# Kernel optimization log

Hardware: AMD Instinct MI355X
Metric: run time of the kernel (lower is better)

The kernel has to match this reference:

```python
import jax, jax.numpy as jnp
import numpy as np

B, N, E = 2, 2048, 1024
H = 16
D = E // H  # head_dim = 64
MLP = 4096
EPS = 1e-5


def _layernorm(x, g, b):
    mu = jnp.mean(x, axis=-1, keepdims=True)
    var = jnp.var(x, axis=-1, keepdims=True)
    return (x - mu) * jax.lax.rsqrt(var + EPS) * g + b


def setup_inputs() -> dict:
    key = jax.random.key(0)
    ks = jax.random.split(key, 12)
    s_e = 1.0 / np.sqrt(E)
    s_m = 1.0 / np.sqrt(MLP)
    return {
        "x": jax.random.normal(ks[0], (B, N, E), jnp.float32),
        "w_qkv": jax.random.uniform(ks[1], (E, 3 * E), jnp.float32, -s_e, s_e),
        "b_qkv": jax.random.uniform(ks[2], (3 * E,), jnp.float32, -s_e, s_e),
        "w_proj": jax.random.uniform(ks[3], (E, E), jnp.float32, -s_e, s_e),
        "b_proj": jax.random.uniform(ks[4], (E,), jnp.float32, -s_e, s_e),
        "g1": jnp.ones((E,), jnp.float32),
        "beta1": jnp.zeros((E,), jnp.float32),
        "g2": jnp.ones((E,), jnp.float32),
        "beta2": jnp.zeros((E,), jnp.float32),
        "w_fc1": jax.random.uniform(ks[5], (E, MLP), jnp.float32, -s_e, s_e),
        "b_fc1": jax.random.uniform(ks[6], (MLP,), jnp.float32, -s_e, s_e),
        "w_fc2": jax.random.uniform(ks[7], (MLP, E), jnp.float32, -s_m, s_m),
        "b_fc2": jax.random.uniform(ks[8], (E,), jnp.float32, -s_m, s_m),
    }


def reference(x, w_qkv, b_qkv, w_proj, b_proj, g1, beta1, g2, beta2,
              w_fc1, b_fc1, w_fc2, b_fc2):
    scale = D ** (-0.5)
    # --- attention block (pre-norm) ---
    h = _layernorm(x, g1, beta1)
    qkv = (h @ w_qkv + b_qkv).reshape(B, N, 3, H, D)
    q, k, v = (qkv[:, :, i].transpose(0, 2, 1, 3) for i in range(3))  # [B,H,N,D]
    scores = jnp.einsum("bhnd,bhmd->bhnm", q, k) * scale  # [B,H,N,N]
    attn = jax.nn.softmax(scores, axis=-1)
    out = jnp.einsum("bhnm,bhmd->bhnd", attn, v)
    out = out.transpose(0, 2, 1, 3).reshape(B, N, E)
    x = x + (out @ w_proj + b_proj)
    # --- MLP block (pre-norm, exact GELU as in torch default) ---
    h = _layernorm(x, g2, beta2)
    h = jax.nn.gelu(h @ w_fc1 + b_fc1, approximate=False) @ w_fc2 + b_fc2
    return x + h
```

## Files before the change

kernel.cpp:

```cpp
#include <hip/hip_runtime.h>
#include <hip/hip_bf16.h>
#include <cmath>


typedef __hip_bfloat16 bf16;
typedef __bf16 bf16x8 __attribute__((ext_vector_type(8)));
typedef __bf16 bf16x4v __attribute__((ext_vector_type(4)));
typedef float  f32x4  __attribute__((ext_vector_type(4)));

#define CB 2
#define CN 2048
#define CE 1024
#define CH 16
#define CD 64
#define CMLP 4096
#define CM (CB*CN)

#define PS 136

__device__ __forceinline__ float b2f(bf16 v){ return __bfloat162float(v); }
__device__ __forceinline__ bf16  f2b(float v){ return __float2bfloat16(v); }

__device__ __forceinline__ void gl_lds16(const void* g, void* l){
  __builtin_amdgcn_global_load_lds((__attribute__((address_space(1))) void*)g,
                                   (__attribute__((address_space(3))) void*)l,
                                   16, 0, 0);
}

__global__ __launch_bounds__(256) void transpose_k(const float* __restrict__ in,
                                                   bf16* __restrict__ out,
                                                   int K, int N){
  __shared__ float tile[32][33];
  const int n0 = blockIdx.x*32, k0 = blockIdx.y*32;
  const int tx = threadIdx.x & 31;
  const int ty = threadIdx.x >> 5;
  #pragma unroll
  for(int i=0;i<32;i+=8) tile[ty+i][tx] = in[(size_t)(k0+ty+i)*N + n0+tx];
  __syncthreads();
  #pragma unroll
  for(int i=0;i<32;i+=8) out[(size_t)(n0+ty+i)*K + k0+tx] = f2b(tile[tx][ty+i]);
}

__global__ __launch_bounds__(256) void ln_k(const float* __restrict__ x,
                                            const float* __restrict__ g,
                                            const float* __restrict__ be,
                                            bf16* __restrict__ out){
  const int row = blockIdx.x;
  const int t = threadIdx.x;
  const float4 v4 = ((const float4*)(x + (size_t)row*CE))[t];
  float v[4] = {v4.x, v4.y, v4.z, v4.w};
  float s=0.f, s2=0.f;
  #pragma unroll
  for(int i=0;i<4;i++){ s+=v[i]; s2+=v[i]*v[i]; }
  #pragma unroll
  for(int off=32; off>0; off>>=1){ s += __shfl_down(s,off); s2 += __shfl_down(s2,off); }
  __shared__ float red[8];
  __shared__ float mu_s, rs_s;
  const int wv=t>>6, ln=t&63;
  if(ln==0){ red[wv]=s; red[4+wv]=s2; }
  __syncthreads();
  if(t==0){
    float S=red[0]+red[1]+red[2]+red[3], S2=red[4]+red[5]+red[6]+red[7];
    float mu=S/CE;
    mu_s=mu; rs_s=rsqrtf(S2/CE - mu*mu + 1e-5f);
  }
  __syncthreads();
  const float mu=mu_s, rs=rs_s;
  #pragma unroll
  for(int i=0;i<4;i++){
    int c=t*4+i;
    out[(size_t)row*CE+c] = f2b((v[i]-mu)*rs*g[c] + be[c]);
  }
}

#define EP_QKV 0
#define EP_RES 1
#define EP_GELU 2

template<int MODE, int BN>
__global__ __launch_bounds__(256,2) void gemm_k(
  const bf16* __restrict__ A, const bf16* __restrict__ BT,
  const float* __restrict__ bias, const float* __restrict__ res,
  float* __restrict__ Cf, bf16* __restrict__ Cb,
  bf16* __restrict__ Cq, bf16* __restrict__ Ck, bf16* __restrict__ Cv,
  int Ksz, int Nsz)
{
  constexpr int NJ = BN/32;
  __shared__ __align__(16) bf16 Alds[2][128*64];
  __shared__ __align__(16) bf16 Blds[2][BN*64];
  const int tid = threadIdx.x;
  const int wave = tid>>6, lane = tid&63;
  const int m16 = lane&15, quad = lane>>4;
  const int wi = wave>>1, wj = wave&1;

  const int lin = blockIdx.x + gridDim.x*blockIdx.y;
  const int m_idx = (lin&7) + 8*((lin>>3)&3);
  const int n_idx = lin>>5;
  const size_t m0 = (size_t)m_idx*128;
  const size_t n0 = (size_t)n_idx*BN;

  f32x4 acc[4][NJ] = {};

  const int srow8 = lane>>3;
  const int schk  = ((lane&7)^srow8)*8;
  const bf16* pA = A  + (m0 + 32*wave      + srow8)*(size_t)Ksz + schk;
  const bf16* pB = BT + (n0 + (BN/4)*wave  + srow8)*(size_t)Ksz + schk;

  auto stage = [&](int buf, const bf16* gA, const bf16* gB){
    bf16* lA = &Alds[buf][wave*2048];
    bf16* lB = &Blds[buf][wave*(BN*16)];
    #pragma unroll
    for(int j=0;j<4;j++)  gl_lds16(gA + (size_t)(j*8)*Ksz, lA + j*512);
    #pragma unroll
    for(int j=0;j<NJ;j++) gl_lds16(gB + (size_t)(j*8)*Ksz, lB + j*512);
  };
  auto compute = [&](int buf){
    #pragma unroll
    for(int w=0;w<2;w++){
      const int sw = (m16&7);
      bf16x8 af[4], bfr[NJ];
      #pragma unroll
      for(int i=0;i<4;i++){
        const int row = wi*64+16*i+m16;
        af[i] = *(const bf16x8*)(&Alds[buf][row*64 + ((w*4+quad)^sw)*8]);
      }
      #pragma unroll
      for(int j=0;j<NJ;j++){
        const int row = wj*(BN/2)+16*j+m16;
        bfr[j] = *(const bf16x8*)(&Blds[buf][row*64 + ((w*4+quad)^sw)*8]);
      }
      #pragma unroll
      for(int i=0;i<4;i++)
        #pragma unroll
        for(int j=0;j<NJ;j++)
          acc[i][j] = __builtin_amdgcn_mfma_f32_16x16x32_bf16(af[i], bfr[j], acc[i][j], 0,0,0);
    }
  };

  const int kIters = Ksz/64;
  stage(0, pA, pB); pA += 64; pB += 64;
  for(int kb=0; kb<kIters; ++kb){
    __syncthreads();
    if(kb+1<kIters){ stage((kb+1)&1, pA, pB); pA += 64; pB += 64; }
    compute(kb&1);
  }

  #pragma unroll
  for(int i=0;i<4;i++){
    #pragma unroll
    for(int j=0;j<NJ;j++){
      const int col = (int)n0 + wj*(BN/2) + 16*j + m16;
      const float bcol = bias[col];
      #pragma unroll
      for(int r=0;r<4;r++){
        const int row = (int)m0 + wi*64 + 16*i + quad*4 + r;
        float v = acc[i][j][r] + bcol;
        if constexpr (MODE==EP_QKV){
          const int b = row>>11, n = row&2047;
          const int which = col>>10, cc = col&1023;
          const int h = cc>>6, d = cc&63;
          if(which==0)      Cq[(((size_t)(b*CH+h))*CN+n)*CD + d] = f2b(v);
          else if(which==1) Ck[(((size_t)(b*CH+h))*CN+n)*CD + d] = f2b(v);
          else              Cv[(((size_t)(b*CH+h))*CD+d)*CN + n] = f2b(v);
        } else if constexpr (MODE==EP_RES){
          v += res[(size_t)row*Nsz+col];
          Cf[(size_t)row*Nsz+col] = v;
        } else {
          v = 0.5f*v*(1.f+erff(v*0.70710678118654752f));
          Cb[(size_t)row*Nsz+col] = f2b(v);
        }
      }
    }
  }
}

__global__ __launch_bounds__(256,2) void attn_k(
  const bf16* __restrict__ Q, const bf16* __restrict__ Kx,
  const bf16* __restrict__ Vt, bf16* __restrict__ O)
{
  const int bh = blockIdx.y;
  const int b = bh>>4, h = bh&15;
  const int tid = threadIdx.x;
  const int wave = tid>>6, lane = tid&63;
  const int m16 = lane&15, quad = lane>>4;
  const int sw = m16&7;
  const int q0 = blockIdx.x*128 + wave*32;

  const bf16* Qb = Q  + (size_t)bh*CN*CD;
  const bf16* Kb = Kx + (size_t)bh*CN*CD;
  const bf16* Vb = Vt + (size_t)bh*CD*CN;

  bf16x8 qf[2][2];
  #pragma unroll
  for(int g=0;g<2;g++){
    const bf16* qp = Qb + (size_t)(q0+g*16+m16)*CD + quad*8;
    qf[g][0] = *(const bf16x8*)(qp);
    qf[g][1] = *(const bf16x8*)(qp + 32);
  }

  float li[2] = {0.f, 0.f};
  f32x4 oacc[2][4] = {};

  __shared__ __align__(16) bf16 Klds[128*64];
  __shared__ __align__(16) bf16 Vlds[64*128];
  __shared__ __align__(16) bf16 Plds[4][32*PS];
  bf16* Pw = &Plds[wave][0];

  const int krow = wave*32 + (lane>>3);
  const int kchk = (lane&7) ^ (lane>>3);
  const bf16* pK = Kb + (size_t)krow*CD + kchk*8;
  const int vrow = wave*16 + (lane>>4);
  const bf16* pV[4];
  #pragma unroll
  for(int j=0;j<4;j++){
    const int ck = (lane&15) ^ ((j*4 + (lane>>4)) & 7);
    pV[j] = Vb + (size_t)(vrow + j*4)*CN + ck*8;
  }
  bf16* lK = Klds + wave*2048;
  bf16* lV = Vlds + wave*2048;

  for(int kt=0; kt<CN; kt+=128){
    __syncthreads();
    #pragma unroll
    for(int j=0;j<4;j++){
      gl_lds16(pK + (size_t)j*8*CD, lK + j*512);
      gl_lds16(pV[j],               lV + j*512);
      pV[j] += 128;
    }
    pK += (size_t)128*CD;
    __syncthreads();

    f32x4 sf0[8], sf1[8];
    #pragma unroll
    for(int f=0;f<8;f++){
      const bf16* kb = Klds + (f*16+m16)*64;
      bf16x8 k0 = *(const bf16x8*)(kb + ((quad   ^ sw)*8));
      bf16x8 k1 = *(const bf16x8*)(kb + (((quad+4)^ sw)*8));
      f32x4 t0 = {}, t1 = {};
      t0 = __builtin_amdgcn_mfma_f32_16x16x32_bf16(k0, qf[0][0], t0, 0,0,0);
      t0 = __builtin_amdgcn_mfma_f32_16x16x32_bf16(k1, qf[0][1], t0, 0,0,0);
      t1 = __builtin_amdgcn_mfma_f32_16x16x32_bf16(k0, qf[1][0], t1, 0,0,0);
      t1 = __builtin_amdgcn_mfma_f32_16x16x32_bf16(k1, qf[1][1], t1, 0,0,0);
      sf0[f]=t0; sf1[f]=t1;
    }
    #pragma unroll
    for(int f=0;f<8;f++){
      bf16x4v p0, p1;
      #pragma unroll
      for(int r=0;r<4;r++){
        float e0 = __expf(sf0[f][r]*0.125f); li[0]+=e0; p0[r]=(__bf16)e0;
        float e1 = __expf(sf1[f][r]*0.125f); li[1]+=e1; p1[r]=(__bf16)e1;
      }
      *(bf16x4v*)(Pw + (size_t)m16*PS       + f*16 + quad*4) = p0;
      *(bf16x4v*)(Pw + (size_t)(16+m16)*PS  + f*16 + quad*4) = p1;
    }
    asm volatile("s_waitcnt lgkmcnt(0)" ::: "memory");
    #pragma unroll
    for(int c=0;c<4;c++){
      const bf16x8 ap0 = *(const bf16x8*)(Pw + (size_t)m16*PS      + c*32 + quad*8);
      const bf16x8 ap1 = *(const bf16x8*)(Pw + (size_t)(16+m16)*PS + c*32 + quad*8);
      #pragma unroll
      for(int dt=0;dt<4;dt++){
        const int d = dt*16+m16;
        bf16x8 bv = *(const bf16x8*)(Vlds + d*128 + (((c*4+quad) ^ sw)*8));
        oacc[0][dt] = __builtin_amdgcn_mfma_f32_16x16x32_bf16(ap0, bv, oacc[0][dt], 0,0,0);
        oacc[1][dt] = __builtin_amdgcn_mfma_f32_16x16x32_bf16(ap1, bv, oacc[1][dt], 0,0,0);
      }
    }
  }
  #pragma unroll
  for(int g=0;g<2;g++){
    li[g] += __shfl_xor(li[g], 16);
    li[g] += __shfl_xor(li[g], 32);
  }
  #pragma unroll
  for(int g=0;g<2;g++){
    float linv[4];
    #pragma unroll
    for(int r=0;r<4;r++) linv[r] = 1.f / __shfl(li[g], quad*4+r);
    #pragma unroll
    for(int dt=0;dt<4;dt++){
      #pragma unroll
      for(int r=0;r<4;r++){
        const int row = q0 + g*16 + quad*4 + r;
        O[((size_t)(b*CN+row))*CE + h*CD + dt*16 + m16] = f2b(oacc[g][dt][r]*linv[r]);
      }
    }
  }
}

extern "C" void kernel_launch(void* const* d_in, const int* in_sizes, int n_in,
                              void* d_out, int out_size, void* d_ws, size_t ws_size,
                              hipStream_t stream)
{
  (void)in_sizes; (void)n_in; (void)out_size; (void)ws_size;
  const float* x     = (const float*)d_in[0];
  const float* w_qkv = (const float*)d_in[1];
  const float* b_qkv = (const float*)d_in[2];
  const float* w_proj= (const float*)d_in[3];
  const float* b_proj= (const float*)d_in[4];
  const float* g1    = (const float*)d_in[5];
  const float* be1   = (const float*)d_in[6];
  const float* g2    = (const float*)d_in[7];
  const float* be2   = (const float*)d_in[8];
  const float* w_fc1 = (const float*)d_in[9];
  const float* b_fc1 = (const float*)d_in[10];
  const float* w_fc2 = (const float*)d_in[11];
  const float* b_fc2 = (const float*)d_in[12];
  float* out = (float*)d_out;

  char* ws = (char*)d_ws;
  size_t off = 0;
  auto alloc = [&](size_t bytes)->char*{
    char* p = ws + off;
    off += (bytes + 255) & ~(size_t)255;
    return p;
  };
  bf16* wqkvT = (bf16*)alloc((size_t)3072*1024*2);
  bf16* wprojT= (bf16*)alloc((size_t)1024*1024*2);
  bf16* wfc1T = (bf16*)alloc((size_t)4096*1024*2);
  bf16* wfc2T = (bf16*)alloc((size_t)1024*4096*2);
  bf16* h1    = (bf16*)alloc((size_t)CM*CE*2);
  bf16* q     = (bf16*)alloc((size_t)CM*CE*2);
  bf16* kk    = (bf16*)alloc((size_t)CM*CE*2);
  bf16* vT    = (bf16*)alloc((size_t)CM*CE*2);
  bf16* aO    = (bf16*)alloc((size_t)CM*CE*2);
  float* x2   = (float*)alloc((size_t)CM*CE*4);
  bf16* hmlp  = q;

  transpose_k<<<dim3(3072/32,1024/32),256,0,stream>>>(w_qkv, wqkvT, 1024,3072);
  transpose_k<<<dim3(1024/32,1024/32),256,0,stream>>>(w_proj, wprojT,1024,1024);
  transpose_k<<<dim3(4096/32,1024/32),256,0,stream>>>(w_fc1, wfc1T, 1024,4096);
  transpose_k<<<dim3(1024/32,4096/32),256,0,stream>>>(w_fc2, wfc2T, 4096,1024);

  ln_k<<<CM,256,0,stream>>>(x, g1, be1, h1);
  gemm_k<EP_QKV,128><<<dim3(3072/128, CM/128),256,0,stream>>>(
      h1, wqkvT, b_qkv, nullptr, nullptr, nullptr, q, kk, vT, 1024, 3072);
  attn_k<<<dim3(CN/128, CB*CH),256,0,stream>>>(q, kk, vT, aO);
  gemm_k<EP_RES,64><<<dim3(1024/64, CM/128),256,0,stream>>>(
      aO, wprojT, b_proj, x, x2, nullptr, nullptr,nullptr,nullptr, 1024, 1024);
  ln_k<<<CM,256,0,stream>>>(x2, g2, be2, h1);
  gemm_k<EP_GELU,128><<<dim3(4096/128, CM/128),256,0,stream>>>(
      h1, wfc1T, b_fc1, nullptr, nullptr, hmlp, nullptr,nullptr,nullptr, 1024, 4096);
  gemm_k<EP_RES,64><<<dim3(1024/64, CM/128),256,0,stream>>>(
      hmlp, wfc2T, b_fc2, x2, out, nullptr, nullptr,nullptr,nullptr, 4096, 1024);
}
```

Measured before the change: 358.5 us.

## Double-buffer attention K/V tiles and parametrize GEMM K-tile depth

The attention kernel now walks keys in 64-wide tiles. K and V are double-buffered in LDS, so the next tile loads while the current one is computed, which removes one of the two barriers per iteration. The P scratch buffer drops its padding in favour of an XOR-swizzled layout to avoid bank conflicts. Separately, the GEMM gains a BK template parameter and the 128-wide GEMMs switch to BK=32, which halves their LDS footprint but doubles the number of k-iterations and barriers.

```diff
diff --git a/kernel.cpp b/kernel.cpp
--- a/kernel.cpp
+++ b/kernel.cpp
@@ -15,8 +15,6 @@
 #define CD 64
 #define CMLP 4096
 #define CM (CB*CN)
-
-#define PS 136
 
 __device__ __forceinline__ float b2f(bf16 v){ return __bfloat162float(v); }
 __device__ __forceinline__ bf16  f2b(float v){ return __float2bfloat16(v); }
@@ -77,7 +75,7 @@
 #define EP_RES 1
 #define EP_GELU 2
 
-template<int MODE, int BN>
+template<int MODE, int BN, int BK>
 __global__ __launch_bounds__(256,2) void gemm_k(
   const bf16* __restrict__ A, const bf16* __restrict__ BT,
   const float* __restrict__ bias, const float* __restrict__ res,
@@ -85,9 +83,13 @@
   bf16* __restrict__ Cq, bf16* __restrict__ Ck, bf16* __restrict__ Cv,
   int Ksz, int Nsz)
 {
-  constexpr int NJ = BN/32;
-  __shared__ __align__(16) bf16 Alds[2][128*64];
-  __shared__ __align__(16) bf16 Blds[2][BN*64];
+  constexpr int NJ  = BN/32;
+  constexpr int CPR = BK/8;
+  constexpr int RPI = 64/CPR;
+  constexpr int AI  = 32/RPI;
+  constexpr int BI  = (BN/4)/RPI;
+  __shared__ __align__(16) bf16 Alds[2][128*BK];
+  __shared__ __align__(16) bf16 Blds[2][BN*BK];
   const int tid = threadIdx.x;
   const int wave = tid>>6, lane = tid&63;
   const int m16 = lane&15, quad = lane>>4;
@@ -101,33 +103,34 @@
 
   f32x4 acc[4][NJ] = {};
 
-  const int srow8 = lane>>3;
-  const int schk  = ((lane&7)^srow8)*8;
-  const bf16* pA = A  + (m0 + 32*wave      + srow8)*(size_t)Ksz + schk;
-  const bf16* pB = BT + (n0 + (BN/4)*wave  + srow8)*(size_t)Ksz + schk;
+  const int srow = lane/CPR;
+  const int schk = ((lane%CPR) ^ (srow&(CPR-1)))*8;
+  const bf16* pA = A  + (m0 + 32*wave      + srow)*(size_t)Ksz + schk;
+  const bf16* pB = BT + (n0 + (BN/4)*wave  + srow)*(size_t)Ksz + schk;
 
   auto stage = [&](int buf, const bf16* gA, const bf16* gB){
-    bf16* lA = &Alds[buf][wave*2048];
-    bf16* lB = &Blds[buf][wave*(BN*16)];
-    #pragma unroll
-    for(int j=0;j<4;j++)  gl_lds16(gA + (size_t)(j*8)*Ksz, lA + j*512);
-    #pragma unroll
-    for(int j=0;j<NJ;j++) gl_lds16(gB + (size_t)(j*8)*Ksz, lB + j*512);
+    bf16* lA = &Alds[buf][wave*(32*BK)];
+    bf16* lB = &Blds[buf][wave*((BN/4)*BK)];
+    #pragma unroll
+    for(int j=0;j<AI;j++) gl_lds16(gA + (size_t)(j*RPI)*Ksz, lA + j*512);
+    #pragma unroll
+    for(int j=0;j<BI;j++) gl_lds16(gB + (size_t)(j*RPI)*Ksz, lB + j*512);
   };
   auto compute = [&](int buf){
-    #pragma unroll
-    for(int w=0;w<2;w++){
-      const int sw = (m16&7);
+    constexpr int NW = BK/32;
+    const int sw = m16&(CPR-1);
+    #pragma unroll
+    for(int w=0;w<NW;w++){
       bf16x8 af[4], bfr[NJ];
       #pragma unroll
       for(int i=0;i<4;i++){
         const int row = wi*64+16*i+m16;
-        af[i] = *(const bf16x8*)(&Alds[buf][row*64 + ((w*4+quad)^sw)*8]);
+        af[i] = *(const bf16x8*)(&Alds[buf][row*BK + ((w*4+quad)^sw)*8]);
       }
       #pragma unroll
       for(int j=0;j<NJ;j++){
         const int row = wj*(BN/2)+16*j+m16;
-        bfr[j] = *(const bf16x8*)(&Blds[buf][row*64 + ((w*4+quad)^sw)*8]);
+        bfr[j] = *(const bf16x8*)(&Blds[buf][row*BK + ((w*4+quad)^sw)*8]);
       }
       #pragma unroll
       for(int i=0;i<4;i++)
@@ -137,11 +140,11 @@
     }
   };
 
-  const int kIters = Ksz/64;
-  stage(0, pA, pB); pA += 64; pB += 64;
+  const int kIters = Ksz/BK;
+  stage(0, pA, pB); pA += BK; pB += BK;
   for(int kb=0; kb<kIters; ++kb){
     __syncthreads();
-    if(kb+1<kIters){ stage((kb+1)&1, pA, pB); pA += 64; pB += 64; }
+    if(kb+1<kIters){ stage((kb+1)&1, pA, pB); pA += BK; pB += BK; }
     compute(kb&1);
   }
 
@@ -201,41 +204,39 @@
   float li[2] = {0.f, 0.f};
   f32x4 oacc[2][4] = {};
 
-  __shared__ __align__(16) bf16 Klds[128*64];
-  __shared__ __align__(16) bf16 Vlds[64*128];
-  __shared__ __align__(16) bf16 Plds[4][32*PS];
+  __shared__ __align__(16) bf16 Klds[2][64*64];
+  __shared__ __align__(16) bf16 Vlds[2][64*64];
+  __shared__ __align__(16) bf16 Plds[4][32*64];
   bf16* Pw = &Plds[wave][0];
 
-  const int krow = wave*32 + (lane>>3);
-  const int kchk = (lane&7) ^ (lane>>3);
-  const bf16* pK = Kb + (size_t)krow*CD + kchk*8;
-  const int vrow = wave*16 + (lane>>4);
-  const bf16* pV[4];
-  #pragma unroll
-  for(int j=0;j<4;j++){
-    const int ck = (lane&15) ^ ((j*4 + (lane>>4)) & 7);
-    pV[j] = Vb + (size_t)(vrow + j*4)*CN + ck*8;
-  }
-  bf16* lK = Klds + wave*2048;
-  bf16* lV = Vlds + wave*2048;
-
-  for(int kt=0; kt<CN; kt+=128){
+  const int srow8 = lane>>3;
+  const int schk  = ((lane&7)^srow8)*8;
+  const bf16* pK = Kb + (size_t)(wave*16 + srow8)*CD + schk;
+  const bf16* pV = Vb + (size_t)(wave*16 + srow8)*CN + schk;
+
+  auto stage = [&](int buf, int kt){
+    bf16* lK = &Klds[buf][wave*1024];
+    bf16* lV = &Vlds[buf][wave*1024];
+    #pragma unroll
+    for(int j=0;j<2;j++){
+      gl_lds16(pK + ((size_t)kt + j*8)*CD, lK + j*512);
+      gl_lds16(pV + (size_t)j*8*CN + kt,   lV + j*512);
+    }
+  };
+
+  stage(0, 0);
+  const int nIter = CN/64;
+  for(int it=0; it<nIter; ++it){
+    const int buf = it&1;
     __syncthreads();
-    #pragma unroll
-    for(int j=0;j<4;j++){
-      gl_lds16(pK + (size_t)j*8*CD, lK + j*512);
-      gl_lds16(pV[j],               lV + j*512);
-      pV[j] += 128;
-    }
-    pK += (size_t)128*CD;
-    __syncthreads();
-
-    f32x4 sf0[8], sf1[8];
-    #pragma unroll
-    for(int f=0;f<8;f++){
-      const bf16* kb = Klds + (f*16+m16)*64;
-      bf16x8 k0 = *(const bf16x8*)(kb + ((quad   ^ sw)*8));
-      bf16x8 k1 = *(const bf16x8*)(kb + (((quad+4)^ sw)*8));
+    if(it+1<nIter) stage(buf^1, (it+1)*64);
+
+    f32x4 sf0[4], sf1[4];
+    #pragma unroll
+    for(int f=0;f<4;f++){
+      const bf16* kb = &Klds[buf][(f*16+m16)*64];
+      bf16x8 k0 = *(const bf16x8*)(kb + ((quad  )^sw)*8);
+      bf16x8 k1 = *(const bf16x8*)(kb + ((quad+4)^sw)*8);
       f32x4 t0 = {}, t1 = {};
       t0 = __builtin_amdgcn_mfma_f32_16x16x32_bf16(k0, qf[0][0], t0, 0,0,0);
       t0 = __builtin_amdgcn_mfma_f32_16x16x32_bf16(k1, qf[0][1], t0, 0,0,0);
@@ -244,25 +245,26 @@
       sf0[f]=t0; sf1[f]=t1;
     }
     #pragma unroll
-    for(int f=0;f<8;f++){
+    for(int f=0;f<4;f++){
       bf16x4v p0, p1;
       #pragma unroll
       for(int r=0;r<4;r++){
         float e0 = __expf(sf0[f][r]*0.125f); li[0]+=e0; p0[r]=(__bf16)e0;
         float e1 = __expf(sf1[f][r]*0.125f); li[1]+=e1; p1[r]=(__bf16)e1;
       }
-      *(bf16x4v*)(Pw + (size_t)m16*PS       + f*16 + quad*4) = p0;
-      *(bf16x4v*)(Pw + (size_t)(16+m16)*PS  + f*16 + quad*4) = p1;
+      const int soff = ((2*f+(quad>>1))^sw)*8 + (quad&1)*4;
+      *(bf16x4v*)(Pw + (m16    )*64 + soff) = p0;
+      *(bf16x4v*)(Pw + (16+m16 )*64 + soff) = p1;
     }
     asm volatile("s_waitcnt lgkmcnt(0)" ::: "memory");
     #pragma unroll
-    for(int c=0;c<4;c++){
-      const bf16x8 ap0 = *(const bf16x8*)(Pw + (size_t)m16*PS      + c*32 + quad*8);
-      const bf16x8 ap1 = *(const bf16x8*)(Pw + (size_t)(16+m16)*PS + c*32 + quad*8);
+    for(int c=0;c<2;c++){
+      const int coff = ((c*4+quad)^sw)*8;
+      const bf16x8 ap0 = *(const bf16x8*)(Pw + (m16   )*64 + coff);
+      const bf16x8 ap1 = *(const bf16x8*)(Pw + (16+m16)*64 + coff);
       #pragma unroll
       for(int dt=0;dt<4;dt++){
-        const int d = dt*16+m16;
-        bf16x8 bv = *(const bf16x8*)(Vlds + d*128 + (((c*4+quad) ^ sw)*8));
+        bf16x8 bv = *(const bf16x8*)(&Vlds[buf][(dt*16+m16)*64 + coff]);
         oacc[0][dt] = __builtin_amdgcn_mfma_f32_16x16x32_bf16(ap0, bv, oacc[0][dt], 0,0,0);
         oacc[1][dt] = __builtin_amdgcn_mfma_f32_16x16x32_bf16(ap1, bv, oacc[1][dt], 0,0,0);
       }
@@ -334,14 +336,14 @@
   transpose_k<<<dim3(1024/32,4096/32),256,0,stream>>>(w_fc2, wfc2T, 4096,1024);
 
   ln_k<<<CM,256,0,stream>>>(x, g1, be1, h1);
-  gemm_k<EP_QKV,128><<<dim3(3072/128, CM/128),256,0,stream>>>(
+  gemm_k<EP_QKV,128,32><<<dim3(3072/128, CM/128),256,0,stream>>>(
       h1, wqkvT, b_qkv, nullptr, nullptr, nullptr, q, kk, vT, 1024, 3072);
   attn_k<<<dim3(CN/128, CB*CH),256,0,stream>>>(q, kk, vT, aO);
-  gemm_k<EP_RES,64><<<dim3(1024/64, CM/128),256,0,stream>>>(
+  gemm_k<EP_RES,64,64><<<dim3(1024/64, CM/128),256,0,stream>>>(
       aO, wprojT, b_proj, x, x2, nullptr, nullptr,nullptr,nullptr, 1024, 1024);
   ln_k<<<CM,256,0,stream>>>(x2, g2, be2, h1);
-  gemm_k<EP_GELU,128><<<dim3(4096/128, CM/128),256,0,stream>>>(
+  gemm_k<EP_GELU,128,32><<<dim3(4096/128, CM/128),256,0,stream>>>(
       h1, wfc1T, b_fc1, nullptr, nullptr, hmlp, nullptr,nullptr,nullptr, 1024, 4096);
-  gemm_k<EP_RES,64><<<dim3(1024/64, CM/128),256,0,stream>>>(
+  gemm_k<EP_RES,64,64><<<dim3(1024/64, CM/128),256,0,stream>>>(
       hmlp, wfc2T, b_fc2, x2, out, nullptr, nullptr,nullptr,nullptr, 4096, 1024);
 }
```

After: 358.3 us. About the same (-0.0%).
